# Optimization experiments

Hardware: AMD Instinct MI355X
Metric: run time of the kernel (lower is better)

Reference implementation:

```python
import jax, jax.numpy as jnp
import numpy as np

N = 100_000   # nodes
E = 1_600_000 # edges
F = 128       # input features
H = 128       # hidden
C = 10        # classes
G = 64        # graphs in batch
NUM_LAYERS = 3


def setup_inputs() -> dict:
    key = jax.random.key(0)
    ks = jax.random.split(key, 16)
    x = jax.random.normal(ks[0], (N, F), jnp.float32)
    edge_index = jax.random.randint(ks[1], (2, E), 0, N, dtype=jnp.int64)
    batch = jnp.sort(jax.random.randint(ks[2], (N,), 0, G, dtype=jnp.int64))
    sF = 1.0 / np.sqrt(F)
    sH = 1.0 / np.sqrt(H)
    return {
        "x": x,
        "edge_index": edge_index,
        "batch": batch,
        # conv1 (main) and convs_random_1 branches
        "W1": jax.random.normal(ks[3], (F, H), jnp.float32) * sF,
        "b1": jnp.zeros((H,), jnp.float32),
        "Wr1": jax.random.normal(ks[4], (F, H), jnp.float32) * sF,
        "br1": jnp.zeros((H,), jnp.float32),
        # num_layers-1 hidden GCNConv layers (distinct weights per layer)
        "W2": jax.random.normal(ks[5], (NUM_LAYERS - 1, H, H), jnp.float32) * sH,
        "b2": jnp.zeros((NUM_LAYERS - 1, H), jnp.float32),
        # single shared random-branch conv for all hidden layers
        "Wr": jax.random.normal(ks[6], (H, H), jnp.float32) * sH,
        "br": jnp.zeros((H,), jnp.float32),
        # readout MLP
        "Wl1": jax.random.normal(ks[7], (H, H), jnp.float32) * sH,
        "bl1": jnp.zeros((H,), jnp.float32),
        "Wl2": jax.random.normal(ks[8], (H, C), jnp.float32) * sH,
        "bl2": jnp.zeros((C,), jnp.float32),
    }


def reference(x, edge_index, batch, W1, b1, Wr1, br1, W2, b2, Wr, br,
              Wl1, bl1, Wl2, bl2):
    src, dst = edge_index[0], edge_index[1]
    # GCN symmetric norm with self-loops: deg = in-degree + 1
    deg = jax.ops.segment_sum(jnp.ones((E,), x.dtype), dst, num_segments=N) + 1.0
    dinv_sqrt = deg ** -0.5
    enorm = (dinv_sqrt[src] * dinv_sqrt[dst])[:, None]   # [E,1]
    self_norm = (1.0 / deg)[:, None]                      # [N,1] self-loop coeff

    def gcn_conv(h, W, b):
        h = h @ W                                         # [N,H]
        agg = jax.ops.segment_sum(h[src] * enorm, dst, num_segments=N)
        return agg + h * self_norm + b

    h = jax.nn.relu(0.95 * gcn_conv(x, W1, b1) + 0.05 * gcn_conv(x, Wr1, br1))
    for i in range(NUM_LAYERS - 1):
        h = jax.nn.relu(0.95 * gcn_conv(h, W2[i], b2[i])
                        + 0.05 * gcn_conv(h, Wr, br))

    # global mean pool over graphs
    counts = jax.ops.segment_sum(jnp.ones((N,), x.dtype), batch, num_segments=G)
    pooled = jax.ops.segment_sum(h, batch, num_segments=G) / jnp.maximum(counts, 1.0)[:, None]

    out = jax.nn.relu(pooled @ Wl1 + bl1)
    # dropout p=0.5 is identity in eval mode
    logits = out @ Wl2 + bl2
    return jax.nn.log_softmax(logits, axis=-1)
```

## Files before the change

kernel.cpp:

```cpp
#include <hip/hip_runtime.h>
#include <hip/hip_bf16.h>
#include <hip/hip_fp8.h>

#define NN 100000
#define NE 1600000
#define FF 128
#define HH 128
#define CC 10
#define GG 64

#define NCHUNK 2048
#define CE 782
#define NBUCKET 128
#define BSPAN 782
#define PSEG 16
#define SRCBITS 17

typedef __attribute__((ext_vector_type(8))) short short8;
typedef __attribute__((ext_vector_type(4))) float f32x4;
typedef __attribute__((ext_vector_type(2))) float f32x2;

__device__ inline unsigned short f2bf(float f) {
    union { float f; unsigned int i; } x;
    x.f = f;
    unsigned int r = x.i + 0x7FFF + ((x.i >> 16) & 1);
    return (unsigned short)(r >> 16);
}
__device__ inline unsigned char f8enc_sw(float v) {
    __hip_fp8_e4m3 q(v);
    return (unsigned char)q.__x;
}
__device__ inline float f8dec(unsigned char b) {
    __hip_fp8_e4m3 q;
    q.__x = (__hip_fp8_storage_t)b;
    return (float)q;
}

#if defined(__has_builtin)
#if __has_builtin(__builtin_amdgcn_cvt_pk_f32_fp8)
#define HAVE_CVT_PK_F32_FP8 1
#endif
#if __has_builtin(__builtin_amdgcn_cvt_pk_fp8_f32)
#define HAVE_CVT_PK_FP8 1
#endif
#endif

__device__ inline void dec8(uint2 v, float* o) {
#ifdef HAVE_CVT_PK_F32_FP8
    f32x2 p;
    p = __builtin_amdgcn_cvt_pk_f32_fp8(v.x, false); o[0] = p[0]; o[1] = p[1];
    p = __builtin_amdgcn_cvt_pk_f32_fp8(v.x, true);  o[2] = p[0]; o[3] = p[1];
    p = __builtin_amdgcn_cvt_pk_f32_fp8(v.y, false); o[4] = p[0]; o[5] = p[1];
    p = __builtin_amdgcn_cvt_pk_f32_fp8(v.y, true);  o[6] = p[0]; o[7] = p[1];
#else
#pragma unroll
    for (int j = 0; j < 4; ++j) {
        o[j]     = f8dec((v.x >> (8 * j)) & 0xFF);
        o[j + 4] = f8dec((v.y >> (8 * j)) & 0xFF);
    }
#endif
}
__device__ inline void dec8p(uint2 v, f32x2* o) {
#ifdef HAVE_CVT_PK_F32_FP8
    o[0] = __builtin_amdgcn_cvt_pk_f32_fp8(v.x, false);
    o[1] = __builtin_amdgcn_cvt_pk_f32_fp8(v.x, true);
    o[2] = __builtin_amdgcn_cvt_pk_f32_fp8(v.y, false);
    o[3] = __builtin_amdgcn_cvt_pk_f32_fp8(v.y, true);
#else
    float d[8]; dec8(v, d);
#pragma unroll
    for (int j = 0; j < 4; ++j) { o[j][0] = d[2 * j]; o[j][1] = d[2 * j + 1]; }
#endif
}
__device__ inline unsigned enc_pk4(float a, float b, float c, float d) {
#ifdef HAVE_CVT_PK_FP8
    int w = __builtin_amdgcn_cvt_pk_fp8_f32(a, b, 0, false);
    w = __builtin_amdgcn_cvt_pk_fp8_f32(c, d, w, true);
    return (unsigned)w;
#else
    return (unsigned)f8enc_sw(a) | ((unsigned)f8enc_sw(b) << 8) |
           ((unsigned)f8enc_sw(c) << 16) | ((unsigned)f8enc_sw(d) << 24);
#endif
}
__device__ inline unsigned char f8enc1(float v) {
#ifdef HAVE_CVT_PK_FP8
    return (unsigned char)(__builtin_amdgcn_cvt_pk_fp8_f32(v, v, 0, false) & 0xFF);
#else
    return f8enc_sw(v);
#endif
}
__device__ inline unsigned pack2bf(float a, float b) {
    return (unsigned)f2bf(a) | ((unsigned)f2bf(b) << 16);
}

__global__ __launch_bounds__(256) void combw_kernel(const float* __restrict__ W1, const float* __restrict__ b1,
                                                    const float* __restrict__ Wr1, const float* __restrict__ br1,
                                                    const float* __restrict__ W2, const float* __restrict__ b2,
                                                    const float* __restrict__ Wr, const float* __restrict__ br,
                                                    unsigned short* __restrict__ Wpack, float* __restrict__ bc) {
    int idx = blockIdx.x * 256 + threadIdx.x;
    if (idx >= 3 * 16384) return;
    int l = idx / 16384, rem = idx % 16384;
    int cb = rem / 2048;
    int kb = (rem / 512) % 4;
    int lane = (rem / 8) % 64;
    int j = rem % 8;
    int k = kb * 32 + (lane >> 4) * 8 + j;
    int c = cb * 16 + (lane & 15);
    int wi = k * HH + c;
    float v = (l == 0) ? 0.95f * W1[wi] + 0.05f * Wr1[wi]
                       : 0.95f * W2[(l - 1) * 16384 + wi] + 0.05f * Wr[wi];
    Wpack[idx] = f2bf(v);
    if (rem < HH) {
        bc[l * HH + rem] = (l == 0) ? 0.95f * b1[rem] + 0.05f * br1[rem]
                                    : 0.95f * b2[(l - 1) * HH + rem] + 0.05f * br[rem];
    }
}

__global__ __launch_bounds__(256) void partA1_kernel(const int* __restrict__ ei,
                                                     int* __restrict__ cc) {
    __shared__ int h[NBUCKET];
    int c = blockIdx.x, t = threadIdx.x;
    if (t < NBUCKET) h[t] = 0;
    __syncthreads();
    int beg = c * CE, end = min(beg + CE, NE);
    for (int e = beg + t; e < end; e += 256)
        atomicAdd(&h[ei[NE + e] / BSPAN], 1);
    __syncthreads();
    if (t < NBUCKET) cc[c * NBUCKET + t] = h[t];
}

__global__ __launch_bounds__(256) void partA2_kernel(int* __restrict__ cc,
                                                     int* __restrict__ tot) {
    __shared__ int sh[256];
    int b = blockIdx.x, t = threadIdx.x;
    int v[8]; int s = 0;
#pragma unroll
    for (int i = 0; i < 8; ++i) { v[i] = cc[(t * 8 + i) * NBUCKET + b]; s += v[i]; }
    sh[t] = s; __syncthreads();
    for (int off = 1; off < 256; off <<= 1) {
        int x = (t >= off) ? sh[t - off] : 0; __syncthreads();
        sh[t] += x; __syncthreads();
    }
    int excl = sh[t] - s;
#pragma unroll
    for (int i = 0; i < 8; ++i) {
        cc[(t * 8 + i) * NBUCKET + b] = excl;
        excl += v[i];
    }
    if (t == 255) tot[b] = sh[255];
}

__global__ __launch_bounds__(256) void partA3_kernel(const int* __restrict__ ei,
                                                     const int* __restrict__ cc,
                                                     const int* __restrict__ tot,
                                                     unsigned* __restrict__ eb32) {
    __shared__ int stot[NBUCKET];
    __shared__ int cur[NBUCKET];
    int c = blockIdx.x, t = threadIdx.x;
    if (t < NBUCKET) stot[t] = tot[t];
    __syncthreads();
    for (int off = 1; off < NBUCKET; off <<= 1) {
        int x = (t < NBUCKET && t >= off) ? stot[t - off] : 0;
        __syncthreads();
        if (t < NBUCKET) stot[t] += x;
        __syncthreads();
    }
    if (t < NBUCKET) cur[t] = (stot[t] - tot[t]) + cc[c * NBUCKET + t];
    __syncthreads();
    int beg = c * CE, end = min(beg + CE, NE);
    for (int e = beg + t; e < end; e += 256) {
        int d = ei[NE + e];
        int s = ei[e];
        int b = d / BSPAN;
        int ld = d - b * BSPAN;
        int p = atomicAdd(&cur[b], 1);
        eb32[p] = (unsigned)s | ((unsigned)ld << SRCBITS);
    }
}

__global__ __launch_bounds__(256) void partB_kernel(const unsigned* __restrict__ eb32,
                                                    const int* __restrict__ tot,
                                                    int* __restrict__ offs,
                                                    float* __restrict__ dinv,
                                                    int* __restrict__ csrc) {
    __shared__ int hcnt[BSPAN];
    __shared__ int lcur[BSPAN];
    __shared__ int sh[256];
    __shared__ int gbase_sh;
    int b = blockIdx.x, t = threadIdx.x;
    int lo = b * BSPAN;
    int span = min(BSPAN, NN - lo);
    if (span <= 0) return;
    for (int i = t; i < span; i += 256) hcnt[i] = 0;
    if (t == 0) {
        int g = 0;
        for (int i = 0; i < b; ++i) g += tot[i];
        gbase_sh = g;
    }
    __syncthreads();
    int gbase = gbase_sh;
    int len = tot[b];
    const unsigned* ebb = eb32 + (size_t)gbase;
    for (int e = t; e < len; e += 256)
        atomicAdd(&hcnt[ebb[e] >> SRCBITS], 1);
    __syncthreads();
    int base = t * 4;
    int v[4]; int s = 0;
#pragma unroll
    for (int j = 0; j < 4; ++j) { int i = base + j; v[j] = (i < span) ? hcnt[i] : 0; s += v[j]; }
    sh[t] = s; __syncthreads();
    for (int off = 1; off < 256; off <<= 1) {
        int x = (t >= off) ? sh[t - off] : 0; __syncthreads();
        sh[t] += x; __syncthreads();
    }
    int excl = sh[t] - s + gbase;
#pragma unroll
    for (int j = 0; j < 4; ++j) {
        int i = base + j;
        if (i < span) {
            offs[lo + i] = excl;
            lcur[i] = excl;
            dinv[lo + i] = rsqrtf((float)v[j] + 1.0f);
            excl += v[j];
        }
    }
    if (b == NBUCKET - 1 && t == 0) offs[NN] = NE;
    __syncthreads();
    for (int e = t; e < len; e += 256) {
        unsigned pr = ebb[e];
        int p = atomicAdd(&lcur[pr >> SRCBITS], 1);
        csrc[p] = (int)(pr & ((1u << SRCBITS) - 1));
    }
}

__global__ __launch_bounds__(256) void gemm_f32_kernel(const float* __restrict__ A,
                                                       const unsigned short* __restrict__ Wp,
                                                       const float* __restrict__ dinv,
                                                       unsigned char* __restrict__ out8,
                                                       int nrows) {
    __shared__ unsigned char f8s[64][128];
    int w = threadIdx.x >> 6;
    int l = threadIdx.x & 63;
    int m0 = blockIdx.x * 64 + w * 16;
    int kg = l >> 4;
    int cl = l & 15;
    int arow = m0 + cl;

    short8 a[4];
    if (arow < nrows) {
        const float4* Ar4 = (const float4*)(A + (size_t)arow * HH);
#pragma unroll
        for (int kb = 0; kb < 4; ++kb) {
            float4 u0 = Ar4[kb * 8 + kg * 2];
            float4 u1 = Ar4[kb * 8 + kg * 2 + 1];
            short8 tt;
            tt[0] = (short)f2bf(u0.x); tt[1] = (short)f2bf(u0.y);
            tt[2] = (short)f2bf(u0.z); tt[3] = (short)f2bf(u0.w);
            tt[4] = (short)f2bf(u1.x); tt[5] = (short)f2bf(u1.y);
            tt[6] = (short)f2bf(u1.z); tt[7] = (short)f2bf(u1.w);
            a[kb] = tt;
        }
    } else {
        short8 z = {};
#pragma unroll
        for (int kb = 0; kb < 4; ++kb) a[kb] = z;
    }

    float dv[4];
#pragma unroll
    for (int r = 0; r < 4; ++r) {
        int orow = m0 + kg * 4 + r;
        dv[r] = (orow < nrows) ? dinv[orow] : 0.f;
    }

#pragma unroll
    for (int cb = 0; cb < 8; ++cb) {
        f32x4 acc = {0.f, 0.f, 0.f, 0.f};
#pragma unroll
        for (int kb = 0; kb < 4; ++kb) {
            short8 b = *(const short8*)(Wp + (size_t)(cb * 4 + kb) * 512 + l * 8);
            acc = __builtin_amdgcn_mfma_f32_16x16x32_bf16(a[kb], b, acc, 0, 0, 0);
        }
#pragma unroll
        for (int r = 0; r < 4; ++r)
            f8s[w * 16 + kg * 4 + r][cb * 16 + cl] = f8enc1(acc[r] * dv[r]);
    }
    __syncthreads();
    int blk0 = blockIdx.x * 64;
    for (int u = threadIdx.x; u < 512; u += 256) {
        int row = u >> 3, c16 = u & 7;
        int grow = blk0 + row;
        if (grow < nrows)
            ((uint4*)out8)[(size_t)grow * 8 + c16] = ((const uint4*)&f8s[row][0])[c16];
    }
}

__global__ __launch_bounds__(256) void agg_gemm_kernel(const unsigned char* __restrict__ t8in,
                                                       const int* __restrict__ offs,
                                                       const int* __restrict__ csrc,
                                                       const float* __restrict__ dinv,
                                                       const float* __restrict__ bias,
                                                       const unsigned short* __restrict__ Wp,
                                                       unsigned char* __restrict__ t8out) {
    __shared__ unsigned char hbuf[32 * 256];
    __shared__ unsigned char f8s[32][128];
    __shared__ float sdinv[32];
    int n0 = blockIdx.x * 32;
    int ln = threadIdx.x >> 3;
    int lane = threadIdx.x & 7;
    int n = n0 + ln;

    int beg = offs[n], end = offs[n + 1];
    const uint4* g16 = (const uint4*)t8in;
    f32x2 acc2[8] = {};
    f32x2 d2[4];
    int e = beg;
    for (; e + 7 < end; e += 8) {
        uint4 v[8];
#pragma unroll
        for (int q = 0; q < 8; ++q)
            v[q] = g16[(size_t)csrc[e + q] * 8 + lane];
#pragma unroll
        for (int q = 0; q < 8; ++q) {
            uint2 a, b;
            a.x = v[q].x; a.y = v[q].y; b.x = v[q].z; b.y = v[q].w;
            dec8p(a, d2);
#pragma unroll
            for (int k = 0; k < 4; ++k) acc2[k] += d2[k];
            dec8p(b, d2);
#pragma unroll
            for (int k = 0; k < 4; ++k) acc2[k + 4] += d2[k];
        }
    }
    for (; e <= end; ++e) {
        int s = (e < end) ? csrc[e] : n;
        uint4 v = g16[(size_t)s * 8 + lane];
        uint2 a, b;
        a.x = v.x; a.y = v.y; b.x = v.z; b.y = v.w;
        dec8p(a, d2);
#pragma unroll
        for (int k = 0; k < 4; ++k) acc2[k] += d2[k];
        dec8p(b, d2);
#pragma unroll
        for (int k = 0; k < 4; ++k) acc2[k + 4] += d2[k];
    }
    float dn = dinv[n];
    if (lane == 0) sdinv[ln] = dn;
    const float4* bv = (const float4*)(bias + lane * 16);
    float bb[16];
    {
        float4 b0 = bv[0], b1 = bv[1], b2 = bv[2], b3 = bv[3];
        bb[0]=b0.x; bb[1]=b0.y; bb[2]=b0.z; bb[3]=b0.w;
        bb[4]=b1.x; bb[5]=b1.y; bb[6]=b1.z; bb[7]=b1.w;
        bb[8]=b2.x; bb[9]=b2.y; bb[10]=b2.z; bb[11]=b2.w;
        bb[12]=b3.x; bb[13]=b3.y; bb[14]=b3.z; bb[15]=b3.w;
    }
    float o[16];
#pragma unroll
    for (int j = 0; j < 16; ++j)
        o[j] = fmaxf(fmaf(acc2[j >> 1][j & 1], dn, bb[j]), 0.f);
    uint4 u0, u1;
    u0.x = pack2bf(o[0], o[1]);  u0.y = pack2bf(o[2], o[3]);
    u0.z = pack2bf(o[4], o[5]);  u0.w = pack2bf(o[6], o[7]);
    u1.x = pack2bf(o[8], o[9]);  u1.y = pack2bf(o[10], o[11]);
    u1.z = pack2bf(o[12], o[13]); u1.w = pack2bf(o[14], o[15]);
    unsigned swz = (unsigned)((ln & 7) << 4);
    unsigned base = (unsigned)ln * 256 + (unsigned)lane * 32;
    *(uint4*)(hbuf + ((base) ^ swz)) = u0;
    *(uint4*)(hbuf + ((base + 16) ^ swz)) = u1;
    __syncthreads();

    int wv = threadIdx.x >> 6;
    int l = threadIdx.x & 63;
    int rt = wv & 1;
    int ch = wv >> 1;
    int kg = l >> 4;
    int cl = l & 15;
    int arow = rt * 16 + cl;
    unsigned rswz = (unsigned)((arow & 7) << 4);
    short8 a[4];
#pragma unroll
    for (int kb = 0; kb < 4; ++kb) {
        unsigned boff = (unsigned)arow * 256 + (unsigned)kb * 64 + (unsigned)kg * 16;
        a[kb] = *(const short8*)(hbuf + (boff ^ rswz));
    }
    float dv[4];
#pragma unroll
    for (int r = 0; r < 4; ++r) dv[r] = sdinv[rt * 16 + kg * 4 + r];
#pragma unroll
    for (int q = 0; q < 4; ++q) {
        int cb = ch * 4 + q;
        f32x4 acc = {0.f, 0.f, 0.f, 0.f};
#pragma unroll
        for (int kb = 0; kb < 4; ++kb) {
            short8 b = *(const short8*)(Wp + (size_t)(cb * 4 + kb) * 512 + l * 8);
            acc = __builtin_amdgcn_mfma_f32_16x16x32_bf16(a[kb], b, acc, 0, 0, 0);
        }
#pragma unroll
        for (int r = 0; r < 4; ++r)
            f8s[rt * 16 + kg * 4 + r][cb * 16 + cl] = f8enc1(acc[r] * dv[r]);
    }
    __syncthreads();
    int row2 = threadIdx.x >> 3, c16 = threadIdx.x & 7;
    ((uint4*)t8out)[(size_t)(n0 + row2) * 8 + c16] = ((const uint4*)&f8s[row2][0])[c16];
}

__global__ __launch_bounds__(256) void agg_relu_kernel(const unsigned char* __restrict__ t8,
                                                       const int* __restrict__ offs,
                                                       const int* __restrict__ csrc,
                                                       const float* __restrict__ dinv,
                                                       const float* __restrict__ bias,
                                                       unsigned char* __restrict__ hOut) {
    int n = blockIdx.x * 32 + (threadIdx.x >> 3);
    if (n >= NN) return;
    int lane = threadIdx.x & 7;
    int beg = offs[n], end = offs[n + 1];
    const uint4* g16 = (const uint4*)t8;
    f32x2 acc2[8] = {};
    f32x2 d2[4];
    int e = beg;
    for (; e + 7 < end; e += 8) {
        uint4 v[8];
#pragma unroll
        for (int q = 0; q < 8; ++q)
            v[q] = g16[(size_t)csrc[e + q] * 8 + lane];
#pragma unroll
        for (int q = 0; q < 8; ++q) {
            uint2 a, b;
            a.x = v[q].x; a.y = v[q].y; b.x = v[q].z; b.y = v[q].w;
            dec8p(a, d2);
#pragma unroll
            for (int k = 0; k < 4; ++k) acc2[k] += d2[k];
            dec8p(b, d2);
#pragma unroll
            for (int k = 0; k < 4; ++k) acc2[k + 4] += d2[k];
        }
    }
    for (; e <= end; ++e) {
        int s = (e < end) ? csrc[e] : n;
        uint4 v = g16[(size_t)s * 8 + lane];
        uint2 a, b;
        a.x = v.x; a.y = v.y; b.x = v.z; b.y = v.w;
        dec8p(a, d2);
#pragma unroll
        for (int k = 0; k < 4; ++k) acc2[k] += d2[k];
        dec8p(b, d2);
#pragma unroll
        for (int k = 0; k < 4; ++k) acc2[k + 4] += d2[k];
    }
    float dn = dinv[n];
    const float4* bv = (const float4*)(bias + lane * 16);
    float bb[16];
    float4 b0 = bv[0], b1 = bv[1], b2 = bv[2], b3 = bv[3];
    bb[0]=b0.x; bb[1]=b0.y; bb[2]=b0.z; bb[3]=b0.w;
    bb[4]=b1.x; bb[5]=b1.y; bb[6]=b1.z; bb[7]=b1.w;
    bb[8]=b2.x; bb[9]=b2.y; bb[10]=b2.z; bb[11]=b2.w;
    bb[12]=b3.x; bb[13]=b3.y; bb[14]=b3.z; bb[15]=b3.w;
    float o[16];
#pragma unroll
    for (int j = 0; j < 16; ++j)
        o[j] = fmaxf(fmaf(acc2[j >> 1][j & 1], dn, bb[j]), 0.f);
    uint4 w;
    w.x = enc_pk4(o[0], o[1], o[2], o[3]);
    w.y = enc_pk4(o[4], o[5], o[6], o[7]);
    w.z = enc_pk4(o[8], o[9], o[10], o[11]);
    w.w = enc_pk4(o[12], o[13], o[14], o[15]);
    ((uint4*)hOut)[(size_t)n * 8 + lane] = w;
}

__global__ __launch_bounds__(256) void poolseg_kernel(const unsigned char* __restrict__ h8,
                                                      const int* __restrict__ batch,
                                                      float* __restrict__ psum_seg) {
    int g = blockIdx.x >> 4;
    int seg = blockIdx.x & (PSEG - 1);
    int t = threadIdx.x;
    int lo = 0, hi = NN;
    while (lo < hi) { int m = (lo + hi) >> 1; if (batch[m] < g) lo = m + 1; else hi = m; }
    int lb = lo;
    lo = 0; hi = NN;
    while (lo < hi) { int m = (lo + hi) >> 1; if (batch[m] <= g) lo = m + 1; else hi = m; }
    int ub = lo;
    int len = ub - lb;
    int b0 = lb + (int)(((long long)len * seg) / PSEG);
    int b1 = lb + (int)(((long long)len * (seg + 1)) / PSEG);

    int fg = t & 15;
    int rg = t >> 4;
    const uint2* gp = (const uint2*)h8;
    f32x2 acc2[4] = {};
    f32x2 d2[4];
    for (int n = b0 + rg; n < b1; n += 16) {
        uint2 v = gp[(size_t)n * 16 + fg];
        dec8p(v, d2);
#pragma unroll
        for (int k = 0; k < 4; ++k) acc2[k] += d2[k];
    }
    __shared__ float red[256][8];
#pragma unroll
    for (int j = 0; j < 8; ++j) red[t][j] = acc2[j >> 1][j & 1];
    __syncthreads();
    for (int off = 8; off >= 1; off >>= 1) {
        if (rg < off) {
#pragma unroll
            for (int j = 0; j < 8; ++j) red[t][j] += red[t + off * 16][j];
        }
        __syncthreads();
    }
    if (t < 16) {
#pragma unroll
        for (int j = 0; j < 8; ++j)
            psum_seg[((size_t)g * PSEG + seg) * HH + t * 8 + j] = red[t][j];
    }
}

__global__ __launch_bounds__(128) void mlp2_kernel(const float* __restrict__ psum_seg,
                                                   const int* __restrict__ batch,
                                                   const float* __restrict__ Wl1,
                                                   const float* __restrict__ bl1,
                                                   const float* __restrict__ Wl2,
                                                   const float* __restrict__ bl2,
                                                   float* __restrict__ out) {
    __shared__ float p[128], o1[128], lg[CC];
    int g = blockIdx.x, t = threadIdx.x;
    int lo = 0, hi = NN;
    while (lo < hi) { int m = (lo + hi) >> 1; if (batch[m] < g) lo = m + 1; else hi = m; }
    int lb = lo;
    lo = 0; hi = NN;
    while (lo < hi) { int m = (lo + hi) >> 1; if (batch[m] <= g) lo = m + 1; else hi = m; }
    int len = lo - lb;
    float a = 0.f;
#pragma unroll
    for (int s = 0; s < PSEG; ++s)
        a += psum_seg[((size_t)g * PSEG + s) * HH + t];
    p[t] = a / fmaxf((float)len, 1.f);
    __syncthreads();
    float acc = bl1[t];
    for (int k = 0; k < HH; ++k) acc = fmaf(p[k], Wl1[k * HH + t], acc);
    o1[t] = fmaxf(acc, 0.f);
    __syncthreads();
    if (t < CC) {
        float a2 = bl2[t];
        for (int j = 0; j < HH; ++j) a2 = fmaf(o1[j], Wl2[j * CC + t], a2);
        lg[t] = a2;
    }
    __syncthreads();
    if (t == 0) {
        float m = lg[0];
        for (int c = 1; c < CC; ++c) m = fmaxf(m, lg[c]);
        float s = 0.f;
        for (int c = 0; c < CC; ++c) s += expf(lg[c] - m);
        float ls = logf(s);
        for (int c = 0; c < CC; ++c) out[g * CC + c] = lg[c] - m - ls;
    }
}

extern "C" void kernel_launch(void* const* d_in, const int* in_sizes, int n_in,
                              void* d_out, int out_size, void* d_ws, size_t ws_size,
                              hipStream_t stream) {
    const float* x   = (const float*)d_in[0];
    const int*   ei  = (const int*)d_in[1];
    const int*   bat = (const int*)d_in[2];
    const float* W1  = (const float*)d_in[3];
    const float* b1  = (const float*)d_in[4];
    const float* Wr1 = (const float*)d_in[5];
    const float* br1 = (const float*)d_in[6];
    const float* W2  = (const float*)d_in[7];
    const float* b2  = (const float*)d_in[8];
    const float* Wr  = (const float*)d_in[9];
    const float* br  = (const float*)d_in[10];
    const float* Wl1 = (const float*)d_in[11];
    const float* bl1 = (const float*)d_in[12];
    const float* Wl2 = (const float*)d_in[13];
    const float* bl2 = (const float*)d_in[14];
    float* out = (float*)d_out;

    char* base = (char*)d_ws;
    size_t off = 0;
    auto alloc = [&](size_t bytes) {
        void* p = base + off;
        off += (bytes + 255) & ~(size_t)255;
        return p;
    };
    unsigned char* t8a  = (unsigned char*)alloc((size_t)NN * HH);
    unsigned char* t8b  = (unsigned char*)alloc((size_t)NN * HH);
    unsigned char* h8   = (unsigned char*)alloc((size_t)NN * HH);
    unsigned* eb32 = (unsigned*)alloc((size_t)NE * 4);
    int*   cc     = (int*)alloc((size_t)NCHUNK * NBUCKET * 4);
    int*   csrc   = (int*)alloc((size_t)NE * 4);
    int*   offs   = (int*)alloc((size_t)(NN + 1) * 4);
    float* dinv   = (float*)alloc((size_t)NN * 4);
    int*   tot    = (int*)alloc(NBUCKET * 4);
    unsigned short* Wpack = (unsigned short*)alloc(3 * 16384 * 2);
    float* bc     = (float*)alloc(3 * HH * 4);
    float* psum_seg = (float*)alloc((size_t)GG * PSEG * HH * 4);
    (void)ws_size; (void)in_sizes; (void)n_in; (void)out_size;

    combw_kernel<<<192, 256, 0, stream>>>(W1, b1, Wr1, br1, W2, b2, Wr, br, Wpack, bc);

    partA1_kernel<<<NCHUNK, 256, 0, stream>>>(ei, cc);
    partA2_kernel<<<NBUCKET, 256, 0, stream>>>(cc, tot);
    partA3_kernel<<<NCHUNK, 256, 0, stream>>>(ei, cc, tot, eb32);
    partB_kernel<<<NBUCKET, 256, 0, stream>>>(eb32, tot, offs, dinv, csrc);

    const int GEMM_BLOCKS = (NN + 63) / 64;
    const int FUSE_BLOCKS = NN / 32;
    gemm_f32_kernel<<<GEMM_BLOCKS, 256, 0, stream>>>(x, Wpack, dinv, t8a, NN);
    agg_gemm_kernel<<<FUSE_BLOCKS, 256, 0, stream>>>(t8a, offs, csrc, dinv, bc,
                                                     Wpack + 16384, t8b);
    agg_gemm_kernel<<<FUSE_BLOCKS, 256, 0, stream>>>(t8b, offs, csrc, dinv, bc + HH,
                                                     Wpack + 2 * 16384, t8a);
    agg_relu_kernel<<<FUSE_BLOCKS, 256, 0, stream>>>(t8a, offs, csrc, dinv, bc + 2 * HH, h8);

    poolseg_kernel<<<GG * PSEG, 256, 0, stream>>>(h8, bat, psum_seg);
    mlp2_kernel<<<GG, 128, 0, stream>>>(psum_seg, bat, Wl1, bl1, Wl2, bl2, out);
}
```

Before: 226.2 us.

## Fuse final aggregation with mean-pool via shared and global atomics

```diff
diff --git a/kernel.cpp b/kernel.cpp
--- a/kernel.cpp
+++ b/kernel.cpp
@@ -13,7 +13,6 @@
 #define CE 782
 #define NBUCKET 128
 #define BSPAN 782
-#define PSEG 16
 #define SRCBITS 17
 
 typedef __attribute__((ext_vector_type(8))) short short8;
@@ -366,9 +365,9 @@
     u1.x = pack2bf(o[8], o[9]);  u1.y = pack2bf(o[10], o[11]);
     u1.z = pack2bf(o[12], o[13]); u1.w = pack2bf(o[14], o[15]);
     unsigned swz = (unsigned)((ln & 7) << 4);
-    unsigned base = (unsigned)ln * 256 + (unsigned)lane * 32;
-    *(uint4*)(hbuf + ((base) ^ swz)) = u0;
-    *(uint4*)(hbuf + ((base + 16) ^ swz)) = u1;
+    unsigned rowbase = (unsigned)ln * 256;
+    *(uint4*)(hbuf + ((rowbase + (unsigned)lane * 16) ^ swz)) = u0;
+    *(uint4*)(hbuf + ((rowbase + 128u + (unsigned)lane * 16) ^ swz)) = u1;
     __syncthreads();
 
     int wv = threadIdx.x >> 6;
@@ -382,7 +381,9 @@
     short8 a[4];
 #pragma unroll
     for (int kb = 0; kb < 4; ++kb) {
-        unsigned boff = (unsigned)arow * 256 + (unsigned)kb * 64 + (unsigned)kg * 16;
+        int m = kb * 4 + kg;
+        unsigned col = (unsigned)((m & 1) * 128 + (m >> 1) * 16);
+        unsigned boff = (unsigned)arow * 256 + col;
         a[kb] = *(const short8*)(hbuf + (boff ^ rswz));
     }
     float dv[4];
@@ -406,15 +407,22 @@
     ((uint4*)t8out)[(size_t)(n0 + row2) * 8 + c16] = ((const uint4*)&f8s[row2][0])[c16];
 }
 
-__global__ __launch_bounds__(256) void agg_relu_kernel(const unsigned char* __restrict__ t8,
+__global__ __launch_bounds__(256) void agg_pool_kernel(const unsigned char* __restrict__ t8,
                                                        const int* __restrict__ offs,
                                                        const int* __restrict__ csrc,
                                                        const float* __restrict__ dinv,
                                                        const float* __restrict__ bias,
-                                                       unsigned char* __restrict__ hOut) {
-    int n = blockIdx.x * 32 + (threadIdx.x >> 3);
-    if (n >= NN) return;
+                                                       const int* __restrict__ batch,
+                                                       float* __restrict__ psum) {
+    __shared__ float pg[2][HH];
+    int n0 = blockIdx.x * 32;
+    int ln = threadIdx.x >> 3;
     int lane = threadIdx.x & 7;
+    int n = n0 + ln;
+
+    pg[threadIdx.x >> 7][threadIdx.x & 127] = 0.f;
+    __syncthreads();
+
     int beg = offs[n], end = offs[n + 1];
     const uint4* g16 = (const uint4*)t8;
     f32x2 acc2[8] = {};
@@ -452,69 +460,40 @@
     float dn = dinv[n];
     const float4* bv = (const float4*)(bias + lane * 16);
     float bb[16];
-    float4 b0 = bv[0], b1 = bv[1], b2 = bv[2], b3 = bv[3];
-    bb[0]=b0.x; bb[1]=b0.y; bb[2]=b0.z; bb[3]=b0.w;
-    bb[4]=b1.x; bb[5]=b1.y; bb[6]=b1.z; bb[7]=b1.w;
-    bb[8]=b2.x; bb[9]=b2.y; bb[10]=b2.z; bb[11]=b2.w;
-    bb[12]=b3.x; bb[13]=b3.y; bb[14]=b3.z; bb[15]=b3.w;
-    float o[16];
-#pragma unroll
-    for (int j = 0; j < 16; ++j)
-        o[j] = fmaxf(fmaf(acc2[j >> 1][j & 1], dn, bb[j]), 0.f);
-    uint4 w;
-    w.x = enc_pk4(o[0], o[1], o[2], o[3]);
-    w.y = enc_pk4(o[4], o[5], o[6], o[7]);
-    w.z = enc_pk4(o[8], o[9], o[10], o[11]);
-    w.w = enc_pk4(o[12], o[13], o[14], o[15]);
-    ((uint4*)hOut)[(size_t)n * 8 + lane] = w;
-}
-
-__global__ __launch_bounds__(256) void poolseg_kernel(const unsigned char* __restrict__ h8,
-                                                      const int* __restrict__ batch,
-                                                      float* __restrict__ psum_seg) {
-    int g = blockIdx.x >> 4;
-    int seg = blockIdx.x & (PSEG - 1);
+    {
+        float4 b0 = bv[0], b1 = bv[1], b2 = bv[2], b3 = bv[3];
+        bb[0]=b0.x; bb[1]=b0.y; bb[2]=b0.z; bb[3]=b0.w;
+        bb[4]=b1.x; bb[5]=b1.y; bb[6]=b1.z; bb[7]=b1.w;
+        bb[8]=b2.x; bb[9]=b2.y; bb[10]=b2.z; bb[11]=b2.w;
+        bb[12]=b3.x; bb[13]=b3.y; bb[14]=b3.z; bb[15]=b3.w;
+    }
+    int g0 = batch[n0];
+    int gn = batch[n];
+    int slot = gn - g0;
+    if (slot <= 1) {
+#pragma unroll
+        for (int j = 0; j < 16; ++j) {
+            float v = fmaxf(fmaf(acc2[j >> 1][j & 1], dn, bb[j]), 0.f);
+            atomicAdd(&pg[slot][lane * 16 + j], v);
+        }
+    } else {
+#pragma unroll
+        for (int j = 0; j < 16; ++j) {
+            float v = fmaxf(fmaf(acc2[j >> 1][j & 1], dn, bb[j]), 0.f);
+            atomicAdd(&psum[(size_t)gn * HH + lane * 16 + j], v);
+        }
+    }
+    __syncthreads();
+    int gEnd = batch[n0 + 31];
     int t = threadIdx.x;
-    int lo = 0, hi = NN;
-    while (lo < hi) { int m = (lo + hi) >> 1; if (batch[m] < g) lo = m + 1; else hi = m; }
-    int lb = lo;
-    lo = 0; hi = NN;
-    while (lo < hi) { int m = (lo + hi) >> 1; if (batch[m] <= g) lo = m + 1; else hi = m; }
-    int ub = lo;
-    int len = ub - lb;
-    int b0 = lb + (int)(((long long)len * seg) / PSEG);
-    int b1 = lb + (int)(((long long)len * (seg + 1)) / PSEG);
-
-    int fg = t & 15;
-    int rg = t >> 4;
-    const uint2* gp = (const uint2*)h8;
-    f32x2 acc2[4] = {};
-    f32x2 d2[4];
-    for (int n = b0 + rg; n < b1; n += 16) {
-        uint2 v = gp[(size_t)n * 16 + fg];
-        dec8p(v, d2);
-#pragma unroll
-        for (int k = 0; k < 4; ++k) acc2[k] += d2[k];
-    }
-    __shared__ float red[256][8];
-#pragma unroll
-    for (int j = 0; j < 8; ++j) red[t][j] = acc2[j >> 1][j & 1];
-    __syncthreads();
-    for (int off = 8; off >= 1; off >>= 1) {
-        if (rg < off) {
-#pragma unroll
-            for (int j = 0; j < 8; ++j) red[t][j] += red[t + off * 16][j];
-        }
-        __syncthreads();
-    }
-    if (t < 16) {
-#pragma unroll
-        for (int j = 0; j < 8; ++j)
-            psum_seg[((size_t)g * PSEG + seg) * HH + t * 8 + j] = red[t][j];
-    }
-}
-
-__global__ __launch_bounds__(128) void mlp2_kernel(const float* __restrict__ psum_seg,
+    if (t < HH) {
+        atomicAdd(&psum[(size_t)g0 * HH + t], pg[0][t]);
+    } else if (gEnd > g0) {
+        atomicAdd(&psum[(size_t)(g0 + 1) * HH + (t - HH)], pg[1][t - HH]);
+    }
+}
+
+__global__ __launch_bounds__(128) void mlp2_kernel(const float* __restrict__ psum,
                                                    const int* __restrict__ batch,
                                                    const float* __restrict__ Wl1,
                                                    const float* __restrict__ bl1,
@@ -529,11 +508,7 @@
     lo = 0; hi = NN;
     while (lo < hi) { int m = (lo + hi) >> 1; if (batch[m] <= g) lo = m + 1; else hi = m; }
     int len = lo - lb;
-    float a = 0.f;
-#pragma unroll
-    for (int s = 0; s < PSEG; ++s)
-        a += psum_seg[((size_t)g * PSEG + s) * HH + t];
-    p[t] = a / fmaxf((float)len, 1.f);
+    p[t] = psum[(size_t)g * HH + t] / fmaxf((float)len, 1.f);
     __syncthreads();
     float acc = bl1[t];
     for (int k = 0; k < HH; ++k) acc = fmaf(p[k], Wl1[k * HH + t], acc);
@@ -584,7 +559,6 @@
     };
     unsigned char* t8a  = (unsigned char*)alloc((size_t)NN * HH);
     unsigned char* t8b  = (unsigned char*)alloc((size_t)NN * HH);
-    unsigned char* h8   = (unsigned char*)alloc((size_t)NN * HH);
     unsigned* eb32 = (unsigned*)alloc((size_t)NE * 4);
     int*   cc     = (int*)alloc((size_t)NCHUNK * NBUCKET * 4);
     int*   csrc   = (int*)alloc((size_t)NE * 4);
@@ -593,8 +567,10 @@
     int*   tot    = (int*)alloc(NBUCKET * 4);
     unsigned short* Wpack = (unsigned short*)alloc(3 * 16384 * 2);
     float* bc     = (float*)alloc(3 * HH * 4);
-    float* psum_seg = (float*)alloc((size_t)GG * PSEG * HH * 4);
+    float* psum   = (float*)alloc((size_t)GG * HH * 4);
     (void)ws_size; (void)in_sizes; (void)n_in; (void)out_size;
+
+    hipMemsetAsync(psum, 0, (size_t)GG * HH * 4, stream);
 
     combw_kernel<<<192, 256, 0, stream>>>(W1, b1, Wr1, br1, W2, b2, Wr, br, Wpack, bc);
 
@@ -610,8 +586,8 @@
                                                      Wpack + 16384, t8b);
     agg_gemm_kernel<<<FUSE_BLOCKS, 256, 0, stream>>>(t8b, offs, csrc, dinv, bc + HH,
                                                      Wpack + 2 * 16384, t8a);
-    agg_relu_kernel<<<FUSE_BLOCKS, 256, 0, stream>>>(t8a, offs, csrc, dinv, bc + 2 * HH, h8);
-
-    poolseg_kernel<<<GG * PSEG, 256, 0, stream>>>(h8, bat, psum_seg);
-    mlp2_kernel<<<GG, 128, 0, stream>>>(psum_seg, bat, Wl1, bl1, Wl2, bl2, out);
-}
+    agg_pool_kernel<<<FUSE_BLOCKS, 256, 0, stream>>>(t8a, offs, csrc, dinv, bc + 2 * HH,
+                                                     bat, psum);
+
+    mlp2_kernel<<<GG, 128, 0, stream>>>(psum, bat, Wl1, bl1, Wl2, bl2, out);
+}
```

Result: slower. 278.5 us (+23.1%).
